# Kernel tuning notes

Hardware: AMD Instinct MI355X
Metric: run time of the kernel (lower is better)

## Reference

```python
import jax, jax.numpy as jnp
import numpy as np
import math

B, L, D, H = 2, 2048, 1024, 16
HD = D // H  # 64
SYNC_THRESHOLD = -0.7
LN_EPS = 1e-12


def setup_inputs() -> dict:
    key = jax.random.key(0)
    ks = jax.random.split(key, 12)
    s = 0.02
    return {
        "hidden_states": jax.random.normal(ks[0], (B, L, D), dtype=jnp.float32),
        "attention_mask": jnp.zeros((B, 1, 1, L), dtype=jnp.float32),
        "phi": jax.random.normal(ks[1], (B, L, H), dtype=jnp.float32),
        "Wq": jax.random.normal(ks[2], (D, D), dtype=jnp.float32) * s,
        "bq": jnp.zeros((D,), dtype=jnp.float32),
        "Wk": jax.random.normal(ks[3], (D, D), dtype=jnp.float32) * s,
        "bk": jnp.zeros((D,), dtype=jnp.float32),
        "Wv": jax.random.normal(ks[4], (D, D), dtype=jnp.float32) * s,
        "bv": jnp.zeros((D,), dtype=jnp.float32),
        "Wo": jax.random.normal(ks[5], (D, D), dtype=jnp.float32) * s,
        "bo": jnp.zeros((D,), dtype=jnp.float32),
        "ln_g": jnp.ones((D,), dtype=jnp.float32),
        "ln_b": jnp.zeros((D,), dtype=jnp.float32),
    }


def _shape(x):  # [B,L,D] -> [B,H,L,HD]
    return x.reshape(B, L, H, HD).transpose(0, 2, 1, 3)


def _rotate_half(x):
    x1, x2 = jnp.split(x, 2, axis=-1)
    return jnp.concatenate([-x2, x1], axis=-1)


def reference(hidden_states, attention_mask, phi, Wq, bq, Wk, bk, Wv, bv, Wo, bo, ln_g, ln_b):
    residual = hidden_states
    q = _shape(hidden_states @ Wq.T + bq)
    k = _shape(hidden_states @ Wk.T + bk)
    v = _shape(hidden_states @ Wv.T + bv)

    # phase per (batch, head, token): [B,H,L,1]; constant across head_dim,
    # so cos/sin of the concatenated phase are the same scalar per token/head.
    p = jnp.transpose(phi, (0, 2, 1))[..., None]
    cos_p = jnp.cos(p)
    sin_p = jnp.sin(p)
    q_rot = q * cos_p + _rotate_half(q) * sin_p
    k_rot = k * cos_p + _rotate_half(k) * sin_p

    scores = jnp.einsum("bhqd,bhkd->bhqk", q_rot, k_rot) / math.sqrt(HD)

    # data-dependent sync mask: mask pairs whose phase difference is anti-synced
    delta_phi = p - jnp.swapaxes(p, -1, -2)           # [B,H,L,L]
    eye = jnp.eye(L, dtype=bool)[None, None]          # [1,1,L,L]
    sync_mask = (jnp.cos(delta_phi) < SYNC_THRESHOLD) & ~eye
    scores = jnp.where(sync_mask, -1e9, scores)
    scores = scores + attention_mask

    # all-masked edge case: zero diagonal score so softmax attends to self
    row_max = jnp.max(scores, axis=-1, keepdims=True)
    all_masked = row_max <= -1e8
    scores = jnp.where(all_masked & eye, 0.0, scores)

    probs = jax.nn.softmax(scores, axis=-1)
    ctx = jnp.einsum("bhqk,bhkd->bhqd", probs, v)
    ctx = ctx.transpose(0, 2, 1, 3).reshape(B, L, D)

    out = ctx @ Wo.T + bo
    x = out + residual
    mean = jnp.mean(x, axis=-1, keepdims=True)
    var = jnp.var(x, axis=-1, keepdims=True)
    return (x - mean) / jnp.sqrt(var + LN_EPS) * ln_g + ln_b
```

## Files before the change

kernel.cpp:

```cpp
#include <hip/hip_runtime.h>
#include <cmath>

#define BB 2
#define LL 2048
#define DD 1024
#define HH 16
#define HDD 64

typedef _Float16 v8h __attribute__((ext_vector_type(8)));
typedef _Float16 v4h __attribute__((ext_vector_type(4)));
typedef _Float16 v2h __attribute__((ext_vector_type(2)));
typedef float v4f __attribute__((ext_vector_type(4)));

#define LOG2E 1.44269504089f
#define NEGB  (-1.442695e9f)

#define GLD(gp, lp)                                                        \
  __builtin_amdgcn_global_load_lds(                                        \
      (const __attribute__((address_space(1))) void*)(gp),                 \
      (__attribute__((address_space(3))) void*)(lp), 16, 0, 0)

__global__ __launch_bounds__(256) void cvt_all(
    const float* __restrict__ hs, const float* __restrict__ wq,
    const float* __restrict__ wk, const float* __restrict__ wv,
    const float* __restrict__ wo, _Float16* __restrict__ hsh,
    _Float16* __restrict__ wqkvh, _Float16* __restrict__ woh)
{
  const int i = blockIdx.x * 256 + threadIdx.x;
  const float* s;
  _Float16* d;
  if (i < 1048576)      { s = hs + (size_t)i * 4;            d = hsh + (size_t)i * 4; }
  else if (i < 1310720) { int j = i - 1048576; s = wq + (size_t)j * 4; d = wqkvh + (size_t)j * 4; }
  else if (i < 1572864) { int j = i - 1310720; s = wk + (size_t)j * 4; d = wqkvh + 1048576 + (size_t)j * 4; }
  else if (i < 1835008) { int j = i - 1572864; s = wv + (size_t)j * 4; d = wqkvh + 2097152 + (size_t)j * 4; }
  else                  { int j = i - 1835008; s = wo + (size_t)j * 4; d = woh + (size_t)j * 4; }
  float4 v = *(const float4*)s;
  v4h o;
  o[0] = (_Float16)v.x; o[1] = (_Float16)v.y;
  o[2] = (_Float16)v.z; o[3] = (_Float16)v.w;
  *(v4h*)d = o;
}

__global__ __launch_bounds__(256) void csgen(
    const float* __restrict__ phi, unsigned* __restrict__ csh2)
{
  const int o = blockIdx.x * 256 + threadIdx.x;
  const int l = o & 2047;
  const int h = (o >> 11) & 15;
  const int b = o >> 15;
  const float ph = phi[(b * 2048 + l) * 16 + h];
  v2h cs;
  cs[0] = (_Float16)cosf(ph);
  cs[1] = (_Float16)sinf(ph);
  csh2[o] = __builtin_bit_cast(unsigned, cs);
}

__device__ __forceinline__ void gemm_loop(
    const _Float16* __restrict__ A, const _Float16* __restrict__ W, const int K,
    const int m0, const int n0, const int tid, const int wave, const int lane,
    _Float16* As, _Float16* Bs, v4f acc[4][4])
{
  const int quad = lane >> 4;
  const int ql = lane & 15;
  const int wm = (wave >> 1) * 64;
  const int wn = (wave & 1) * 64;
  const int srow = tid >> 2;
  const int skof = (tid & 3) * 8;
  const _Float16* Ap = A + (size_t)(m0 + srow) * K + skof;
  const _Float16* Wp = W + (size_t)(n0 + srow) * K + skof;
  const size_t rstep = (size_t)64 * K;
  for (int k0 = 0; k0 < K; k0 += 32) {
    __syncthreads();
    GLD(Ap + k0,         As + tid * 8);
    GLD(Ap + rstep + k0, As + 2048 + tid * 8);
    GLD(Wp + k0,         Bs + tid * 8);
    GLD(Wp + rstep + k0, Bs + 2048 + tid * 8);
    __syncthreads();
    v8h af[4], bf[4];
#pragma unroll
    for (int mt = 0; mt < 4; ++mt)
      af[mt] = *(const v8h*)&As[(wm + mt * 16 + ql) * 32 + quad * 8];
#pragma unroll
    for (int nt = 0; nt < 4; ++nt)
      bf[nt] = *(const v8h*)&Bs[(wn + nt * 16 + ql) * 32 + quad * 8];
#pragma unroll
    for (int mt = 0; mt < 4; ++mt)
#pragma unroll
      for (int nt = 0; nt < 4; ++nt)
        acc[mt][nt] = __builtin_amdgcn_mfma_f32_16x16x32_f16(
            af[mt], bf[nt], acc[mt][nt], 0, 0, 0);
  }
}

__global__ __launch_bounds__(256) void gemm_qkv(
    const _Float16* __restrict__ A, const _Float16* __restrict__ W,
    const float* __restrict__ bqp, const float* __restrict__ bkp,
    const float* __restrict__ bvp, const unsigned* __restrict__ csh2,
    _Float16* __restrict__ qh, _Float16* __restrict__ kh,
    _Float16* __restrict__ vt2)
{
  __shared__ _Float16 As[128 * 32];
  __shared__ _Float16 Bs[128 * 32];
  const int tid = threadIdx.x, lane = tid & 63, wave = tid >> 6;
  const int quad = lane >> 4, ql = lane & 15;
  const int m0 = blockIdx.y * 128, n0 = blockIdx.x * 128;
  v4f acc[4][4];
#pragma unroll
  for (int mt = 0; mt < 4; ++mt)
#pragma unroll
    for (int nt = 0; nt < 4; ++nt) acc[mt][nt] = (v4f){0.f, 0.f, 0.f, 0.f};
  gemm_loop(A, W, DD, m0, n0, tid, wave, lane, As, Bs, acc);

  const int buf = n0 >> 10;
  const int col0 = (n0 & 1023) + (wave & 1) * 64;
  const int hh = col0 >> 6;
  const int mr0 = m0 + (wave >> 1) * 64;

  if (buf == 2) {
    float bb4[4];
#pragma unroll
    for (int nt = 0; nt < 4; ++nt) bb4[nt] = bvp[col0 + nt * 16 + ql];
#pragma unroll
    for (int mt = 0; mt < 4; ++mt) {
      const int row = mr0 + mt * 16 + quad * 4;
      const int b_ = row >> 11;
      const int l = row & 2047;
      _Float16* dst = vt2 + ((size_t)(b_ * 16 + hh) * 32 + (l >> 6)) * 4096 +
                      ((l >> 2) & 15) * 256;
#pragma unroll
      for (int nt = 0; nt < 4; ++nt) {
        const int d = nt * 16 + ql;
        v4h o4;
#pragma unroll
        for (int r = 0; r < 4; ++r) o4[r] = (_Float16)(acc[mt][nt][r] + bb4[nt]);
        *(v4h*)&dst[d * 4] = o4;
      }
    }
  } else {
    const float scl = (buf == 0) ? 0.125f * LOG2E : 1.0f;
    _Float16* outp = (buf == 0) ? qh : kh;
    const float* bias = (buf == 0) ? bqp : bkp;
    float bb4[4];
#pragma unroll
    for (int nt = 0; nt < 4; ++nt) bb4[nt] = bias[col0 + nt * 16 + ql];
#pragma unroll
    for (int mt = 0; mt < 4; ++mt)
#pragma unroll
      for (int r = 0; r < 4; ++r) {
        const int row = mr0 + mt * 16 + quad * 4 + r;
        const int b_ = row >> 11;
        const int l = row & 2047;
        const v2h c2 = __builtin_bit_cast(
            v2h, csh2[(b_ * 16 + hh) * 2048 + l]);
        const float c = (float)c2[0], s = (float)c2[1];
        _Float16* orow = outp + (size_t)row * DD + col0 + ql;
#pragma unroll
        for (int pp = 0; pp < 2; ++pp) {
          const float a0 = acc[mt][pp][r] + bb4[pp];
          const float a1 = acc[mt][pp + 2][r] + bb4[pp + 2];
          orow[pp * 16]        = (_Float16)((a0 * c - a1 * s) * scl);
          orow[(pp + 2) * 16]  = (_Float16)((a1 * c + a0 * s) * scl);
        }
      }
  }
}

__global__ __launch_bounds__(256) void gemm_o(
    const _Float16* __restrict__ A, const _Float16* __restrict__ W,
    const float* __restrict__ bo, const float* __restrict__ res,
    float* __restrict__ out)
{
  __shared__ _Float16 As[128 * 32];
  __shared__ _Float16 Bs[128 * 32];
  const int tid = threadIdx.x, lane = tid & 63, wave = tid >> 6;
  const int quad = lane >> 4, ql = lane & 15;
  const int m0 = blockIdx.y * 128, n0 = blockIdx.x * 128;
  v4f acc[4][4];
#pragma unroll
  for (int mt = 0; mt < 4; ++mt)
#pragma unroll
    for (int nt = 0; nt < 4; ++nt) acc[mt][nt] = (v4f){0.f, 0.f, 0.f, 0.f};
  gemm_loop(A, W, DD, m0, n0, tid, wave, lane, As, Bs, acc);
  const int nc0 = n0 + (wave & 1) * 64;
  const int mr0 = m0 + (wave >> 1) * 64;
#pragma unroll
  for (int nt = 0; nt < 4; ++nt) {
    const int col = nc0 + nt * 16 + ql;
    const float bb = bo[col];
#pragma unroll
    for (int mt = 0; mt < 4; ++mt)
#pragma unroll
      for (int r = 0; r < 4; ++r) {
        const int row = mr0 + mt * 16 + quad * 4 + r;
        const size_t ix = (size_t)row * DD + col;
        out[ix] = acc[mt][nt][r] + bb + res[ix];
      }
  }
}

__global__ __launch_bounds__(256) void attn_db(
    const _Float16* __restrict__ Q, const _Float16* __restrict__ K,
    const _Float16* __restrict__ VT2, const unsigned* __restrict__ csh2,
    const float* __restrict__ am, _Float16* __restrict__ ctx)
{
  __shared__ _Float16 Kt[2][4096];
  __shared__ _Float16 Vt[2][4096];
  __shared__ float amL[LL];

  const int tid  = threadIdx.x;
  const int lane = tid & 63;
  const int wave = tid >> 6;
  const int quad = lane >> 4;
  const int ql   = lane & 15;
  const int bid  = blockIdx.x;
  const int bh = bid & 31;
  const int qt = bid >> 5;
  const int h  = bh & 15;
  const int b  = bh >> 4;
  const int q0w = qt * 64 + wave * 16;
  const int qglob = q0w + ql;
  const int csb = bh * LL;

  {
    const float* amb = am + b * LL;
    for (int i = tid; i < LL; i += 256) amL[i] = amb[i] * LOG2E;
  }

  v8h qf[2];
  {
    const _Float16* qp = Q + ((size_t)(b * LL + qglob)) * DD + h * 64 + quad * 8;
    qf[0] = *(const v8h*)qp;
    qf[1] = *(const v8h*)(qp + 32);
  }
  v4h bq = (v4h){0, 0, 0, 0};
  {
    const v2h c2 = __builtin_bit_cast(v2h, csh2[csb + qglob]);
    if (quad == 0) { bq[0] = c2[0]; bq[1] = c2[1]; }
  }
  const v4h ones = (v4h){(_Float16)1.f, (_Float16)1.f,
                         (_Float16)1.f, (_Float16)1.f};

  v4f o[4];
#pragma unroll
  for (int nt = 0; nt < 4; ++nt) o[nt] = (v4f){0.f, 0.f, 0.f, 0.f};
  v4f lacc = (v4f){0.f, 0.f, 0.f, 0.f};

  const _Float16* Kb   = K + (size_t)(b * LL) * DD + h * 64;
  const _Float16* VTb2 = VT2 + (size_t)bh * 131072;
  const unsigned* csk = csh2 + csb;

  const int srow = tid >> 3;
  const int kch  = (tid & 7) ^ (srow & 7);

  {
    const size_t kg = (size_t)srow * 1024 + kch * 8;
    GLD(Kb + kg,             &Kt[0][tid * 8]);
    GLD(Kb + kg + 32 * 1024, &Kt[0][2048 + tid * 8]);
    GLD(VTb2 + tid * 8,          &Vt[0][tid * 8]);
    GLD(VTb2 + 2048 + tid * 8,   &Vt[0][2048 + tid * 8]);
  }
  unsigned cs_cur[4], cs_nxt[4];
#pragma unroll
  for (int c = 0; c < 4; ++c) cs_cur[c] = csk[c * 16 + ql];
  __syncthreads();

  for (int t = 0; t < 32; ++t) {
    const int k0 = t * 64;
    const int buf = t & 1;
    if (t < 31) {
      const int k1 = k0 + 64;
      const size_t kg = (size_t)(k1 + srow) * 1024 + kch * 8;
      GLD(Kb + kg,             &Kt[buf ^ 1][tid * 8]);
      GLD(Kb + kg + 32 * 1024, &Kt[buf ^ 1][2048 + tid * 8]);
      const _Float16* vsrc = VTb2 + (size_t)(t + 1) * 4096;
      GLD(vsrc + tid * 8,        &Vt[buf ^ 1][tid * 8]);
      GLD(vsrc + 2048 + tid * 8, &Vt[buf ^ 1][2048 + tid * 8]);
#pragma unroll
      for (int c = 0; c < 4; ++c) cs_nxt[c] = csk[k1 + c * 16 + ql];
    }
    const _Float16* KtB = Kt[buf];
    const _Float16* VtB = Vt[buf];

    v4f st[4], dd[4];
#pragma unroll
    for (int c = 0; c < 4; ++c) {
      const int row = c * 16 + ql;
      const int sw = row & 7;
      v8h a0 = *(const v8h*)&KtB[row * 64 + ((quad ^ sw) << 3)];
      v8h a1 = *(const v8h*)&KtB[row * 64 + (((quad + 4) ^ sw) << 3)];
      v4f z = (v4f){0.f, 0.f, 0.f, 0.f};
      z = __builtin_amdgcn_mfma_f32_16x16x32_f16(a0, qf[0], z, 0, 0, 0);
      z = __builtin_amdgcn_mfma_f32_16x16x32_f16(a1, qf[1], z, 0, 0, 0);
      st[c] = z;
      const v2h c2 = __builtin_bit_cast(v2h, cs_cur[c]);
      v4h a = (v4h){0, 0, 0, 0};
      if (quad == 0) { a[0] = c2[0]; a[1] = c2[1]; }
      dd[c] = __builtin_amdgcn_mfma_f32_16x16x16f16(
          a, bq, (v4f){0.f, 0.f, 0.f, 0.f}, 0, 0, 0);
    }

    v4h pf[4];
    const bool hasdiag = ((unsigned)(q0w - k0)) < 64u;
    if (hasdiag) {
#pragma unroll
      for (int c = 0; c < 4; ++c) {
        const v4f am4 = *(const v4f*)&amL[k0 + c * 16 + quad * 4];
        float p[4];
#pragma unroll
        for (int r = 0; r < 4; ++r) {
          const bool msk = (dd[c][r] < -0.7f) &&
                           ((k0 + c * 16 + quad * 4 + r) != qglob);
          p[r] = __builtin_amdgcn_exp2f((msk ? NEGB : st[c][r]) + am4[r]);
        }
        const unsigned u01 = __builtin_bit_cast(
            unsigned, __builtin_amdgcn_cvt_pkrtz(p[0], p[1]));
        const unsigned u23 = __builtin_bit_cast(
            unsigned, __builtin_amdgcn_cvt_pkrtz(p[2], p[3]));
        pf[c] = __builtin_bit_cast(v4h, make_uint2(u01, u23));
      }
    } else {
#pragma unroll
      for (int c = 0; c < 4; ++c) {
        const v4f am4 = *(const v4f*)&amL[k0 + c * 16 + quad * 4];
        float p[4];
#pragma unroll
        for (int r = 0; r < 4; ++r) {
          p[r] = __builtin_amdgcn_exp2f(
              ((dd[c][r] < -0.7f) ? NEGB : st[c][r]) + am4[r]);
        }
        const unsigned u01 = __builtin_bit_cast(
            unsigned, __builtin_amdgcn_cvt_pkrtz(p[0], p[1]));
        const unsigned u23 = __builtin_bit_cast(
            unsigned, __builtin_amdgcn_cvt_pkrtz(p[2], p[3]));
        pf[c] = __builtin_bit_cast(v4h, make_uint2(u01, u23));
      }
    }

#pragma unroll
    for (int c = 0; c < 4; ++c) {
      lacc = __builtin_amdgcn_mfma_f32_16x16x16f16(pf[c], ones, lacc, 0, 0, 0);
#pragma unroll
      for (int nt = 0; nt < 4; ++nt) {
        const v4h vv = *(const v4h*)&VtB[((c * 4 + quad) * 64 +
                                          nt * 16 + ql) * 4];
        o[nt] = __builtin_amdgcn_mfma_f32_16x16x16f16(pf[c], vv, o[nt], 0, 0, 0);
      }
    }
#pragma unroll
    for (int c = 0; c < 4; ++c) cs_cur[c] = cs_nxt[c];
    __syncthreads();
  }

#pragma unroll
  for (int r = 0; r < 4; ++r) {
    const int q = q0w + quad * 4 + r;
    const float lr = lacc[r];
    const size_t ob = (size_t)(b * LL + q) * DD + h * 64 + ql;
    if (lr <= 0.f) {
      const _Float16* vsrc = VTb2 + (q >> 6) * 4096 +
                             ((q >> 2) & 15) * 256 + (q & 3);
#pragma unroll
      for (int nt = 0; nt < 4; ++nt)
        ctx[ob + nt * 16] = vsrc[(nt * 16 + ql) * 4];
    } else {
      const float inv = 1.f / lr;
      ctx[ob + 0]  = (_Float16)(o[0][r] * inv);
      ctx[ob + 16] = (_Float16)(o[1][r] * inv);
      ctx[ob + 32] = (_Float16)(o[2][r] * inv);
      ctx[ob + 48] = (_Float16)(o[3][r] * inv);
    }
  }
}

__global__ __launch_bounds__(256) void layernorm(
    const float* __restrict__ x, const float* __restrict__ g,
    const float* __restrict__ bta, float* __restrict__ out)
{
  __shared__ float red[8];
  const int row = blockIdx.x;
  const int tid = threadIdx.x;
  const float* xr = x + (size_t)row * DD;
  float lsum = 0.f, lsq = 0.f;
  float v[4];
#pragma unroll
  for (int i = 0; i < 4; ++i) {
    v[i] = xr[tid + i * 256];
    lsum += v[i];
    lsq += v[i] * v[i];
  }
#pragma unroll
  for (int off = 32; off > 0; off >>= 1) {
    lsum += __shfl_down(lsum, off, 64);
    lsq  += __shfl_down(lsq,  off, 64);
  }
  const int wid = tid >> 6;
  if ((tid & 63) == 0) { red[wid] = lsum; red[wid + 4] = lsq; }
  __syncthreads();
  const float tsum = red[0] + red[1] + red[2] + red[3];
  const float tsq  = red[4] + red[5] + red[6] + red[7];
  const float mean = tsum * (1.f / DD);
  const float var  = tsq * (1.f / DD) - mean * mean;
  const float inv  = rsqrtf(var + 1e-12f);
#pragma unroll
  for (int i = 0; i < 4; ++i) {
    const int c = tid + i * 256;
    out[(size_t)row * DD + c] = (v[i] - mean) * inv * g[c] + bta[c];
  }
}

extern "C" void kernel_launch(void* const* d_in, const int* in_sizes, int n_in,
                              void* d_out, int out_size, void* d_ws, size_t ws_size,
                              hipStream_t stream)
{
  const float* hs  = (const float*)d_in[0];
  const float* amk = (const float*)d_in[1];
  const float* phi = (const float*)d_in[2];
  const float* Wq  = (const float*)d_in[3];
  const float* bq  = (const float*)d_in[4];
  const float* Wk  = (const float*)d_in[5];
  const float* bk  = (const float*)d_in[6];
  const float* Wv  = (const float*)d_in[7];
  const float* bv  = (const float*)d_in[8];
  const float* Wo  = (const float*)d_in[9];
  const float* bo  = (const float*)d_in[10];
  const float* lng = (const float*)d_in[11];
  const float* lnb = (const float*)d_in[12];
  float* out = (float*)d_out;

  const size_t SZ = (size_t)BB * LL * DD;
  _Float16* hsh   = (_Float16*)d_ws;
  _Float16* qh    = hsh + SZ;
  _Float16* kh    = qh + SZ;
  _Float16* vt2   = kh + SZ;
  _Float16* ctxh  = vt2 + SZ;
  _Float16* wqkvh = ctxh + SZ;
  _Float16* woh   = wqkvh + 3 * (size_t)DD * DD;
  float* xb    = (float*)(woh + (size_t)DD * DD);
  unsigned* csh2 = (unsigned*)(xb + SZ);

  cvt_all<<<8192, 256, 0, stream>>>(hs, Wq, Wk, Wv, Wo, hsh, wqkvh, woh);
  csgen<<<256, 256, 0, stream>>>(phi, csh2);
  gemm_qkv<<<dim3(24, 32), 256, 0, stream>>>(hsh, wqkvh, bq, bk, bv, csh2,
                                             qh, kh, vt2);
  attn_db<<<1024, 256, 0, stream>>>(qh, kh, vt2, csh2, amk, ctxh);
  gemm_o<<<dim3(8, 32), 256, 0, stream>>>(ctxh, woh, bo, hs, xb);
  layernorm<<<BB * LL, 256, 0, stream>>>(xb, lng, lnb, out);
}
```

Before: 248.9 us.

## Triple-buffer K tiles in attention, precompute mask scale, shrink output GEMM tile

The attention kernel now triple-buffers K tiles and issues them two iterations ahead. It replaces the full __syncthreads with explicit vmcnt waits plus s_barrier, so loads overlap compute with finer-grained synchronisation. The attention mask scaling moves into the csgen kernel and is read per tile from global into registers, which frees the 8KB shared amL array and allows a 4-blocks-per-SM launch bound. The output projection GEMM uses 128x64 tiles with its own inline loop, doubling the grid for better occupancy. The trade-offs are more register pressure and fragile hand-written waitcnt logic.

```diff
diff --git a/kernel.cpp b/kernel.cpp
--- a/kernel.cpp
+++ b/kernel.cpp
@@ -42,9 +42,11 @@
 }
 
 __global__ __launch_bounds__(256) void csgen(
-    const float* __restrict__ phi, unsigned* __restrict__ csh2)
+    const float* __restrict__ phi, const float* __restrict__ amk,
+    unsigned* __restrict__ csh2, float* __restrict__ aml2)
 {
   const int o = blockIdx.x * 256 + threadIdx.x;
+  if (o < BB * LL) aml2[o] = amk[o] * LOG2E;
   const int l = o & 2047;
   const int h = (o >> 11) & 15;
   const int b = o >> 15;
@@ -171,41 +173,64 @@
     float* __restrict__ out)
 {
   __shared__ _Float16 As[128 * 32];
-  __shared__ _Float16 Bs[128 * 32];
+  __shared__ _Float16 Bs[64 * 32];
   const int tid = threadIdx.x, lane = tid & 63, wave = tid >> 6;
   const int quad = lane >> 4, ql = lane & 15;
-  const int m0 = blockIdx.y * 128, n0 = blockIdx.x * 128;
-  v4f acc[4][4];
+  const int m0 = blockIdx.y * 128, n0 = blockIdx.x * 64;
+  v4f acc[4][2];
 #pragma unroll
   for (int mt = 0; mt < 4; ++mt)
 #pragma unroll
-    for (int nt = 0; nt < 4; ++nt) acc[mt][nt] = (v4f){0.f, 0.f, 0.f, 0.f};
-  gemm_loop(A, W, DD, m0, n0, tid, wave, lane, As, Bs, acc);
-  const int nc0 = n0 + (wave & 1) * 64;
-  const int mr0 = m0 + (wave >> 1) * 64;
-#pragma unroll
-  for (int nt = 0; nt < 4; ++nt) {
-    const int col = nc0 + nt * 16 + ql;
+    for (int nt = 0; nt < 2; ++nt) acc[mt][nt] = (v4f){0.f, 0.f, 0.f, 0.f};
+  const int wm = (wave >> 1) * 64;
+  const int wn = (wave & 1) * 32;
+  const int srow = tid >> 2;
+  const int skof = (tid & 3) * 8;
+  const _Float16* Ap = A + (size_t)(m0 + srow) * DD + skof;
+  const _Float16* Wp = W + (size_t)(n0 + srow) * DD + skof;
+  const size_t rstep = (size_t)64 * DD;
+  for (int k0 = 0; k0 < DD; k0 += 32) {
+    __syncthreads();
+    GLD(Ap + k0,         As + tid * 8);
+    GLD(Ap + rstep + k0, As + 2048 + tid * 8);
+    GLD(Wp + k0,         Bs + tid * 8);
+    __syncthreads();
+    v8h af[4], bf[2];
+#pragma unroll
+    for (int mt = 0; mt < 4; ++mt)
+      af[mt] = *(const v8h*)&As[(wm + mt * 16 + ql) * 32 + quad * 8];
+#pragma unroll
+    for (int nt = 0; nt < 2; ++nt)
+      bf[nt] = *(const v8h*)&Bs[(wn + nt * 16 + ql) * 32 + quad * 8];
+#pragma unroll
+    for (int mt = 0; mt < 4; ++mt)
+#pragma unroll
+      for (int nt = 0; nt < 2; ++nt)
+        acc[mt][nt] = __builtin_amdgcn_mfma_f32_16x16x32_f16(
+            af[mt], bf[nt], acc[mt][nt], 0, 0, 0);
+  }
+#pragma unroll
+  for (int nt = 0; nt < 2; ++nt) {
+    const int col = n0 + wn + nt * 16 + ql;
     const float bb = bo[col];
 #pragma unroll
     for (int mt = 0; mt < 4; ++mt)
 #pragma unroll
       for (int r = 0; r < 4; ++r) {
-        const int row = mr0 + mt * 16 + quad * 4 + r;
+        const int row = m0 + wm + mt * 16 + quad * 4 + r;
         const size_t ix = (size_t)row * DD + col;
         out[ix] = acc[mt][nt][r] + bb + res[ix];
       }
   }
 }
 
-__global__ __launch_bounds__(256) void attn_db(
+__global__ __launch_bounds__(256, 4) void attn_db(
     const _Float16* __restrict__ Q, const _Float16* __restrict__ K,
     const _Float16* __restrict__ VT2, const unsigned* __restrict__ csh2,
-    const float* __restrict__ am, _Float16* __restrict__ ctx)
-{
-  __shared__ _Float16 Kt[2][4096];
+    const float* __restrict__ aml2, _Float16* __restrict__ ctx)
+{
+  __shared__ _Float16 Kt[3][4096];
   __shared__ _Float16 Vt[2][4096];
-  __shared__ float amL[LL];
 
   const int tid  = threadIdx.x;
   const int lane = tid & 63;
@@ -221,11 +246,6 @@
   const int qglob = q0w + ql;
   const int csb = bh * LL;
 
-  {
-    const float* amb = am + b * LL;
-    for (int i = tid; i < LL; i += 256) amL[i] = amb[i] * LOG2E;
-  }
-
   v8h qf[2];
   {
     const _Float16* qp = Q + ((size_t)(b * LL + qglob)) * DD + h * 64 + quad * 8;
@@ -248,38 +268,56 @@
   const _Float16* Kb   = K + (size_t)(b * LL) * DD + h * 64;
   const _Float16* VTb2 = VT2 + (size_t)bh * 131072;
   const unsigned* csk = csh2 + csb;
+  const float* amb = aml2 + b * LL;
 
   const int srow = tid >> 3;
   const int kch  = (tid & 7) ^ (srow & 7);
+  const size_t kgb = (size_t)srow * 1024 + kch * 8;
 
   {
-    const size_t kg = (size_t)srow * 1024 + kch * 8;
-    GLD(Kb + kg,             &Kt[0][tid * 8]);
-    GLD(Kb + kg + 32 * 1024, &Kt[0][2048 + tid * 8]);
-    GLD(VTb2 + tid * 8,          &Vt[0][tid * 8]);
-    GLD(VTb2 + 2048 + tid * 8,   &Vt[0][2048 + tid * 8]);
+    GLD(Kb + kgb,             &Kt[0][tid * 8]);
+    GLD(Kb + kgb + 32 * 1024, &Kt[0][2048 + tid * 8]);
+    GLD(VTb2 + tid * 8,           &Vt[0][tid * 8]);
+    GLD(VTb2 + 2048 + tid * 8,    &Vt[0][2048 + tid * 8]);
+    GLD(Kb + kgb + 64 * 1024, &Kt[1][tid * 8]);
+    GLD(Kb + kgb + 96 * 1024, &Kt[1][2048 + tid * 8]);
   }
   unsigned cs_cur[4], cs_nxt[4];
-#pragma unroll
-  for (int c = 0; c < 4; ++c) cs_cur[c] = csk[c * 16 + ql];
-  __syncthreads();
-
+  v4f am_cur[4], am_nxt[4];
+#pragma unroll
+  for (int c = 0; c < 4; ++c) {
+    cs_cur[c] = csk[c * 16 + ql];
+    am_cur[c] = *(const v4f*)&amb[c * 16 + quad * 4];
+  }
+  __builtin_amdgcn_sched_barrier(0);
+  asm volatile("s_waitcnt vmcnt(2)" ::: "memory");
+  __builtin_amdgcn_sched_barrier(0);
+  __builtin_amdgcn_s_barrier();
+  __builtin_amdgcn_sched_barrier(0);
+
+  int kc = 0;
   for (int t = 0; t < 32; ++t) {
     const int k0 = t * 64;
-    const int buf = t & 1;
+    const int vb = t & 1;
     if (t < 31) {
       const int k1 = k0 + 64;
-      const size_t kg = (size_t)(k1 + srow) * 1024 + kch * 8;
-      GLD(Kb + kg,             &Kt[buf ^ 1][tid * 8]);
-      GLD(Kb + kg + 32 * 1024, &Kt[buf ^ 1][2048 + tid * 8]);
+#pragma unroll
+      for (int c = 0; c < 4; ++c) {
+        cs_nxt[c] = csk[k1 + c * 16 + ql];
+        am_nxt[c] = *(const v4f*)&amb[k1 + c * 16 + quad * 4];
+      }
       const _Float16* vsrc = VTb2 + (size_t)(t + 1) * 4096;
-      GLD(vsrc + tid * 8,        &Vt[buf ^ 1][tid * 8]);
-      GLD(vsrc + 2048 + tid * 8, &Vt[buf ^ 1][2048 + tid * 8]);
-#pragma unroll
-      for (int c = 0; c < 4; ++c) cs_nxt[c] = csk[k1 + c * 16 + ql];
-    }
-    const _Float16* KtB = Kt[buf];
-    const _Float16* VtB = Vt[buf];
+      GLD(vsrc + tid * 8,        &Vt[vb ^ 1][tid * 8]);
+      GLD(vsrc + 2048 + tid * 8, &Vt[vb ^ 1][2048 + tid * 8]);
+      if (t < 30) {
+        const int kn = (kc == 0) ? 2 : kc - 1;
+        const size_t kg = kgb + (size_t)(k0 + 128) * 1024;
+        GLD(Kb + kg,             &Kt[kn][tid * 8]);
+        GLD(Kb + kg + 32 * 1024, &Kt[kn][2048 + tid * 8]);
+      }
+    }
+    const _Float16* KtB = Kt[kc];
+    const _Float16* VtB = Vt[vb];
 
     v4f st[4], dd[4];
 #pragma unroll
@@ -304,13 +342,12 @@
     if (hasdiag) {
 #pragma unroll
       for (int c = 0; c < 4; ++c) {
-        const v4f am4 = *(const v4f*)&amL[k0 + c * 16 + quad * 4];
         float p[4];
 #pragma unroll
         for (int r = 0; r < 4; ++r) {
           const bool msk = (dd[c][r] < -0.7f) &&
                            ((k0 + c * 16 + quad * 4 + r) != qglob);
-          p[r] = __builtin_amdgcn_exp2f((msk ? NEGB : st[c][r]) + am4[r]);
+          p[r] = __builtin_amdgcn_exp2f((msk ? NEGB : st[c][r]) + am_cur[c][r]);
         }
         const unsigned u01 = __builtin_bit_cast(
             unsigned, __builtin_amdgcn_cvt_pkrtz(p[0], p[1]));
@@ -321,12 +358,11 @@
     } else {
 #pragma unroll
       for (int c = 0; c < 4; ++c) {
-        const v4f am4 = *(const v4f*)&amL[k0 + c * 16 + quad * 4];
         float p[4];
 #pragma unroll
         for (int r = 0; r < 4; ++r) {
           p[r] = __builtin_amdgcn_exp2f(
-              ((dd[c][r] < -0.7f) ? NEGB : st[c][r]) + am4[r]);
+              ((dd[c][r] < -0.7f) ? NEGB : st[c][r]) + am_cur[c][r]);
         }
         const unsigned u01 = __builtin_bit_cast(
             unsigned, __builtin_amdgcn_cvt_pkrtz(p[0], p[1]));
@@ -346,9 +382,21 @@
         o[nt] = __builtin_amdgcn_mfma_f32_16x16x16f16(pf[c], vv, o[nt], 0, 0, 0);
       }
     }
-#pragma unroll
-    for (int c = 0; c < 4; ++c) cs_cur[c] = cs_nxt[c];
-    __syncthreads();
+
+    if (t < 31) {
+#pragma unroll
+      for (int c = 0; c < 4; ++c) {
+        cs_cur[c] = cs_nxt[c];
+        am_cur[c] = am_nxt[c];
+      }
+      __builtin_amdgcn_sched_barrier(0);
+      if (t < 30) asm volatile("s_waitcnt vmcnt(2)" ::: "memory");
+      else        asm volatile("s_waitcnt vmcnt(0)" ::: "memory");
+      __builtin_amdgcn_sched_barrier(0);
+      __builtin_amdgcn_s_barrier();
+      __builtin_amdgcn_sched_barrier(0);
+    }
+    kc = (kc == 2) ? 0 : kc + 1;
   }
 
 #pragma unroll
@@ -437,12 +485,13 @@
   _Float16* woh   = wqkvh + 3 * (size_t)DD * DD;
   float* xb    = (float*)(woh + (size_t)DD * DD);
   unsigned* csh2 = (unsigned*)(xb + SZ);
+  float* aml2 = (float*)(csh2 + (size_t)BB * HH * LL);
 
   cvt_all<<<8192, 256, 0, stream>>>(hs, Wq, Wk, Wv, Wo, hsh, wqkvh, woh);
-  csgen<<<256, 256, 0, stream>>>(phi, csh2);
+  csgen<<<256, 256, 0, stream>>>(phi, amk, csh2, aml2);
   gemm_qkv<<<dim3(24, 32), 256, 0, stream>>>(hsh, wqkvh, bq, bk, bv, csh2,
                                              qh, kh, vt2);
-  attn_db<<<1024, 256, 0, stream>>>(qh, kh, vt2, csh2, amk, ctxh);
-  gemm_o<<<dim3(8, 32), 256, 0, stream>>>(ctxh, woh, bo, hs, xb);
+  attn_db<<<1024, 256, 0, stream>>>(qh, kh, vt2, csh2, aml2, ctxh);
+  gemm_o<<<dim3(16, 32), 256, 0, stream>>>(ctxh, woh, bo, hs, xb);
   layernorm<<<BB * LL, 256, 0, stream>>>(xb, lng, lnb, out);
 }
```

Result: faster. 242.7 us (-2.5%).

## Retile output GEMM to 128x64 and fold attention mask into MFMA accumulator

Applied to the files above, without the earlier changes.

The output projection GEMM now uses 128x64 tiles with its own inline K loop, doubling the grid from 256 to 512 blocks so more of the device's compute units are occupied. In attention, the additive mask is pre-scaled by log2e once in csgen, then loaded as the initial value of the QK MFMA accumulator, which removes a separate add per score. The diagonal special-case branch is dropped, relying on the diagonal phase difference never crossing the sync threshold. The new GEMM loop is single-buffered with unswizzled shared memory reads, which may cost some load latency and bank conflicts.

```diff
diff --git a/kernel.cpp b/kernel.cpp
--- a/kernel.cpp
+++ b/kernel.cpp
@@ -42,9 +42,11 @@
 }
 
 __global__ __launch_bounds__(256) void csgen(
-    const float* __restrict__ phi, unsigned* __restrict__ csh2)
+    const float* __restrict__ phi, const float* __restrict__ amk,
+    unsigned* __restrict__ csh2, float* __restrict__ aml2)
 {
   const int o = blockIdx.x * 256 + threadIdx.x;
+  if (o < BB * LL) aml2[o] = amk[o] * LOG2E;
   const int l = o & 2047;
   const int h = (o >> 11) & 15;
   const int b = o >> 15;
@@ -171,27 +173,51 @@
     float* __restrict__ out)
 {
   __shared__ _Float16 As[128 * 32];
-  __shared__ _Float16 Bs[128 * 32];
+  __shared__ _Float16 Bs[64 * 32];
   const int tid = threadIdx.x, lane = tid & 63, wave = tid >> 6;
   const int quad = lane >> 4, ql = lane & 15;
-  const int m0 = blockIdx.y * 128, n0 = blockIdx.x * 128;
-  v4f acc[4][4];
+  const int m0 = blockIdx.y * 128, n0 = blockIdx.x * 64;
+  v4f acc[4][2];
 #pragma unroll
   for (int mt = 0; mt < 4; ++mt)
 #pragma unroll
-    for (int nt = 0; nt < 4; ++nt) acc[mt][nt] = (v4f){0.f, 0.f, 0.f, 0.f};
-  gemm_loop(A, W, DD, m0, n0, tid, wave, lane, As, Bs, acc);
-  const int nc0 = n0 + (wave & 1) * 64;
-  const int mr0 = m0 + (wave >> 1) * 64;
-#pragma unroll
-  for (int nt = 0; nt < 4; ++nt) {
-    const int col = nc0 + nt * 16 + ql;
+    for (int nt = 0; nt < 2; ++nt) acc[mt][nt] = (v4f){0.f, 0.f, 0.f, 0.f};
+  const int wm = (wave >> 1) * 64;
+  const int wn = (wave & 1) * 32;
+  const int srow = tid >> 2;
+  const int skof = (tid & 3) * 8;
+  const _Float16* Ap = A + (size_t)(m0 + srow) * DD + skof;
+  const _Float16* Wp = W + (size_t)(n0 + srow) * DD + skof;
+  const size_t rstep = (size_t)64 * DD;
+  for (int k0 = 0; k0 < DD; k0 += 32) {
+    __syncthreads();
+    GLD(Ap + k0,         As + tid * 8);
+    GLD(Ap + rstep + k0, As + 2048 + tid * 8);
+    GLD(Wp + k0,         Bs + tid * 8);
+    __syncthreads();
+    v8h af[4], bf[2];
+#pragma unroll
+    for (int mt = 0; mt < 4; ++mt)
+      af[mt] = *(const v8h*)&As[(wm + mt * 16 + ql) * 32 + quad * 8];
+#pragma unroll
+    for (int nt = 0; nt < 2; ++nt)
+      bf[nt] = *(const v8h*)&Bs[(wn + nt * 16 + ql) * 32 + quad * 8];
+#pragma unroll
+    for (int mt = 0; mt < 4; ++mt)
+#pragma unroll
+      for (int nt = 0; nt < 2; ++nt)
+        acc[mt][nt] = __builtin_amdgcn_mfma_f32_16x16x32_f16(
+            af[mt], bf[nt], acc[mt][nt], 0, 0, 0);
+  }
+#pragma unroll
+  for (int nt = 0; nt < 2; ++nt) {
+    const int col = n0 + wn + nt * 16 + ql;
     const float bb = bo[col];
 #pragma unroll
     for (int mt = 0; mt < 4; ++mt)
 #pragma unroll
       for (int r = 0; r < 4; ++r) {
-        const int row = mr0 + mt * 16 + quad * 4 + r;
+        const int row = m0 + wm + mt * 16 + quad * 4 + r;
         const size_t ix = (size_t)row * DD + col;
         out[ix] = acc[mt][nt][r] + bb + res[ix];
       }
@@ -201,7 +227,7 @@
 __global__ __launch_bounds__(256) void attn_db(
     const _Float16* __restrict__ Q, const _Float16* __restrict__ K,
     const _Float16* __restrict__ VT2, const unsigned* __restrict__ csh2,
-    const float* __restrict__ am, _Float16* __restrict__ ctx)
+    const float* __restrict__ aml2, _Float16* __restrict__ ctx)
 {
   __shared__ _Float16 Kt[2][4096];
   __shared__ _Float16 Vt[2][4096];
@@ -222,8 +248,8 @@
   const int csb = bh * LL;
 
   {
-    const float* amb = am + b * LL;
-    for (int i = tid; i < LL; i += 256) amL[i] = amb[i] * LOG2E;
+    const float* amb = aml2 + b * LL;
+    for (int i = tid; i < LL; i += 256) amL[i] = amb[i];
   }
 
   v8h qf[2];
@@ -288,7 +314,7 @@
       const int sw = row & 7;
       v8h a0 = *(const v8h*)&KtB[row * 64 + ((quad ^ sw) << 3)];
       v8h a1 = *(const v8h*)&KtB[row * 64 + (((quad + 4) ^ sw) << 3)];
-      v4f z = (v4f){0.f, 0.f, 0.f, 0.f};
+      v4f z = *(const v4f*)&amL[k0 + c * 16 + quad * 4];
       z = __builtin_amdgcn_mfma_f32_16x16x32_f16(a0, qf[0], z, 0, 0, 0);
       z = __builtin_amdgcn_mfma_f32_16x16x32_f16(a1, qf[1], z, 0, 0, 0);
       st[c] = z;
@@ -300,40 +326,17 @@
     }
 
     v4h pf[4];
-    const bool hasdiag = ((unsigned)(q0w - k0)) < 64u;
-    if (hasdiag) {
-#pragma unroll
-      for (int c = 0; c < 4; ++c) {
-        const v4f am4 = *(const v4f*)&amL[k0 + c * 16 + quad * 4];
-        float p[4];
-#pragma unroll
-        for (int r = 0; r < 4; ++r) {
-          const bool msk = (dd[c][r] < -0.7f) &&
-                           ((k0 + c * 16 + quad * 4 + r) != qglob);
-          p[r] = __builtin_amdgcn_exp2f((msk ? NEGB : st[c][r]) + am4[r]);
-        }
-        const unsigned u01 = __builtin_bit_cast(
-            unsigned, __builtin_amdgcn_cvt_pkrtz(p[0], p[1]));
-        const unsigned u23 = __builtin_bit_cast(
-            unsigned, __builtin_amdgcn_cvt_pkrtz(p[2], p[3]));
-        pf[c] = __builtin_bit_cast(v4h, make_uint2(u01, u23));
-      }
-    } else {
-#pragma unroll
-      for (int c = 0; c < 4; ++c) {
-        const v4f am4 = *(const v4f*)&amL[k0 + c * 16 + quad * 4];
-        float p[4];
-#pragma unroll
-        for (int r = 0; r < 4; ++r) {
-          p[r] = __builtin_amdgcn_exp2f(
-              ((dd[c][r] < -0.7f) ? NEGB : st[c][r]) + am4[r]);
-        }
-        const unsigned u01 = __builtin_bit_cast(
-            unsigned, __builtin_amdgcn_cvt_pkrtz(p[0], p[1]));
-        const unsigned u23 = __builtin_bit_cast(
-            unsigned, __builtin_amdgcn_cvt_pkrtz(p[2], p[3]));
-        pf[c] = __builtin_bit_cast(v4h, make_uint2(u01, u23));
-      }
+#pragma unroll
+    for (int c = 0; c < 4; ++c) {
+      float p[4];
+#pragma unroll
+      for (int r = 0; r < 4; ++r)
+        p[r] = __builtin_amdgcn_exp2f((dd[c][r] < -0.7f) ? NEGB : st[c][r]);
+      const unsigned u01 = __builtin_bit_cast(
+          unsigned, __builtin_amdgcn_cvt_pkrtz(p[0], p[1]));
+      const unsigned u23 = __builtin_bit_cast(
+          unsigned, __builtin_amdgcn_cvt_pkrtz(p[2], p[3]));
+      pf[c] = __builtin_bit_cast(v4h, make_uint2(u01, u23));
     }
 
 #pragma unroll
@@ -437,12 +440,13 @@
   _Float16* woh   = wqkvh + 3 * (size_t)DD * DD;
   float* xb    = (float*)(woh + (size_t)DD * DD);
   unsigned* csh2 = (unsigned*)(xb + SZ);
+  float* aml2 = (float*)(csh2 + (size_t)BB * HH * LL);
 
   cvt_all<<<8192, 256, 0, stream>>>(hs, Wq, Wk, Wv, Wo, hsh, wqkvh, woh);
-  csgen<<<256, 256, 0, stream>>>(phi, csh2);
+  csgen<<<256, 256, 0, stream>>>(phi, amk, csh2, aml2);
   gemm_qkv<<<dim3(24, 32), 256, 0, stream>>>(hsh, wqkvh, bq, bk, bv, csh2,
                                              qh, kh, vt2);
-  attn_db<<<1024, 256, 0, stream>>>(qh, kh, vt2, csh2, amk, ctxh);
-  gemm_o<<<dim3(8, 32), 256, 0, stream>>>(ctxh, woh, bo, hs, xb);
+  attn_db<<<1024, 256, 0, stream>>>(qh, kh, vt2, csh2, aml2, ctxh);
+  gemm_o<<<dim3(16, 32), 256, 0, stream>>>(ctxh, woh, bo, hs, xb);
   layernorm<<<BB * LL, 256, 0, stream>>>(xb, lng, lnb, out);
 }
```

Result: faster. 240.3 us (-3.5%).
